# Performance work log

Measured on AMD Instinct MI355X. Metric: run time of the kernel, lower is better.

The kernel has to match this reference:

```python
import jax, jax.numpy as jnp
import numpy as np

B, T, C, H = 4, 2048, 768, 12
D = C // H  # head dim = 64


def setup_inputs() -> dict:
    key = jax.random.key(0)
    k1, k2, k3, k4 = jax.random.split(key, 4)
    x = jax.random.normal(k1, (B, T, C), dtype=jnp.float32)
    attn_mask = jnp.ones((B, T), dtype=jnp.float32)
    layer_lambda = jax.random.uniform(k2, (H,), dtype=jnp.float32)
    W_attn = jax.random.normal(k3, (C, 3 * C), dtype=jnp.float32) * (1.0 / np.sqrt(C))
    W_proj = jax.random.normal(k4, (C, C), dtype=jnp.float32) * (1.0 / np.sqrt(C))
    return {"x": x, "attn_mask": attn_mask, "layer_lambda": layer_lambda,
            "W_attn": W_attn, "W_proj": W_proj}


def reference(x, attn_mask, layer_lambda, W_attn, W_proj):
    Bx, Tx, Cx = x.shape
    qkv = x @ W_attn                      # (B, T, 3C)
    q, k, v = jnp.split(qkv, 3, axis=2)
    # (B, H, T, D)
    q = q.reshape(Bx, Tx, H, D).transpose(0, 2, 1, 3)
    k = k.reshape(Bx, Tx, H, D).transpose(0, 2, 1, 3)
    v = v.reshape(Bx, Tx, H, D).transpose(0, 2, 1, 3)

    att = jnp.einsum('bhqd,bhkd->bhqk', q, k) / jnp.sqrt(jnp.float32(D))

    # log-scale bias: scale row q of scores by (1 + lambda_h * log(q+1))
    log_pos = jnp.log(jnp.arange(Tx, dtype=jnp.float32) + 1.0)  # (T,)
    scale = 1.0 + layer_lambda[None, :, None, None] * log_pos[None, None, :, None]
    att = att * scale

    causal = jnp.tril(jnp.ones((Tx, Tx), dtype=jnp.float32))            # (T, T)
    mask = causal[None, None, :, :] * attn_mask[:, None, None, :]       # (B,1,T,T)

    # relu_attention path: relu, mask, normalize by row sum
    att = jax.nn.relu(att) * mask
    att_weights = att / (att.sum(axis=-1, keepdims=True) + 1e-9)

    out = jnp.einsum('bhqk,bhkd->bhqd', att_weights, v)  # (B, H, T, D)
    out = out.transpose(0, 2, 1, 3).reshape(Bx, Tx, Cx)
    return out @ W_proj
```

## Files before the change

kernel.cpp:

```cpp
#include <hip/hip_runtime.h>
#include <cstddef>
#include <cstdint>

#define Bn 4
#define Tn 2048
#define Cn 768
#define Hn 12

typedef __attribute__((ext_vector_type(8))) short short8v;
typedef __attribute__((ext_vector_type(4))) float f32x4;
typedef unsigned short ushort_t;

struct us4 { unsigned short x, y, z, w; };

__device__ inline unsigned short f2bf(float f) {
  union { float f; unsigned u; } v; v.f = f;
  unsigned r = v.u + 0x7FFFu + ((v.u >> 16) & 1u);
  return (unsigned short)(r >> 16);
}
__device__ inline float bf2f(unsigned short u) {
  union { unsigned u; float f; } v; v.u = ((unsigned)u) << 16;
  return v.f;
}
__device__ inline unsigned cvt_pk_bf16(float lo, float hi) {
  unsigned r;
  asm("v_cvt_pk_bf16_f32 %0, %1, %2" : "=v"(r) : "v"(lo), "v"(hi));
  return r;
}

#define GLOAD_LDS16(gp, lp)                                                        \
  __builtin_amdgcn_global_load_lds(                                                \
      (const __attribute__((address_space(1))) void*)(gp),                         \
      (__attribute__((address_space(3))) void*)(lp), 16, 0, 0)

__global__ __launch_bounds__(256) void prep_all(
    const float* __restrict__ x, ushort_t* __restrict__ xh, ushort_t* __restrict__ xl,
    const float* __restrict__ Wa, ushort_t* __restrict__ WaTh,
    ushort_t* __restrict__ WaTl, const float* __restrict__ Wp,
    ushort_t* __restrict__ WpT) {
  __shared__ float t[64][65];
  const int blk = blockIdx.x;
  const int tid = threadIdx.x;
  if (blk < 6144) {
    const int i = blk * 256 + tid;
    float4 v = reinterpret_cast<const float4*>(x)[i];
    us4 h;
    h.x = f2bf(v.x); h.y = f2bf(v.y); h.z = f2bf(v.z); h.w = f2bf(v.w);
    reinterpret_cast<us4*>(xh)[i] = h;
    const int row = (i << 2) / Cn;
    if ((row & (Tn - 1)) < 256) {
      us4 l;
      l.x = f2bf(v.x - bf2f(h.x)); l.y = f2bf(v.y - bf2f(h.y));
      l.z = f2bf(v.z - bf2f(h.z)); l.w = f2bf(v.w - bf2f(h.w));
      reinterpret_cast<us4*>(xl)[i] = l;
    }
    return;
  }
  const int id2 = blk - 6144;
  const int cx  = id2 % 48;
  const int ry  = id2 / 48;
  const bool split = (cx < 36);
  const float* W = split ? Wa : Wp;
  ushort_t* WTh  = split ? WaTh : WpT;
  const int cols = split ? 3 * Cn : Cn;
  const int c0   = (split ? cx : (cx - 36)) * 64;
  const int r0   = ry * 64;
  const int rows = Cn;
  const int c4 = (tid & 15) << 2;
  #pragma unroll
  for (int rr = 0; rr < 4; ++rr) {
    int r = rr * 16 + (tid >> 4);
    float4 v = *reinterpret_cast<const float4*>(&W[(size_t)(r0 + r) * cols + c0 + c4]);
    t[r][c4] = v.x; t[r][c4 + 1] = v.y; t[r][c4 + 2] = v.z; t[r][c4 + 3] = v.w;
  }
  __syncthreads();
  const int r4 = (tid & 15) << 2;
  #pragma unroll
  for (int cc = 0; cc < 4; ++cc) {
    int c = cc * 16 + (tid >> 4);
    float v0 = t[r4][c], v1 = t[r4 + 1][c], v2 = t[r4 + 2][c], v3 = t[r4 + 3][c];
    us4 h;
    h.x = f2bf(v0); h.y = f2bf(v1); h.z = f2bf(v2); h.w = f2bf(v3);
    *reinterpret_cast<us4*>(&WTh[(size_t)(c0 + c) * rows + r0 + r4]) = h;
    if (split) {
      us4 l;
      l.x = f2bf(v0 - bf2f(h.x)); l.y = f2bf(v1 - bf2f(h.y));
      l.z = f2bf(v2 - bf2f(h.z)); l.w = f2bf(v3 - bf2f(h.w));
      *reinterpret_cast<us4*>(&WaTl[(size_t)(c0 + c) * rows + r0 + r4]) = l;
    }
  }
}

__global__ __launch_bounds__(256) void gemm_qkv_fused(
    const ushort_t* __restrict__ Ah, const ushort_t* __restrict__ Al,
    const ushort_t* __restrict__ Bh, const ushort_t* __restrict__ Bl,
    const float* __restrict__ lambda, const float* __restrict__ attn_mask,
    ushort_t* __restrict__ qhp, ushort_t* __restrict__ qlp,
    ushort_t* __restrict__ khp, ushort_t* __restrict__ klp,
    ushort_t* __restrict__ vtp) {
  constexpr int K = Cn, N = 3 * Cn;
  __shared__ ushort_t As[2][128 * 64];
  __shared__ ushort_t Bs[2][128 * 64];

  const int tid = threadIdx.x;
  const int w = tid >> 6;
  const int lane = tid & 63;
  const int lcol = lane & 15;
  const int g = lane >> 4;
  const int xcd = blockIdx.x & 7;
  const int pos = blockIdx.x >> 3;
  const bool comp = (pos < 12);
  int bm, bn;
  if (comp) {
    const int cid = xcd * 12 + pos;
    bm = (xcd >> 1) * Tn + (xcd & 1) * 128;
    bn = (cid % 12) * 128;
  } else {
    const int pid = xcd * 144 + (pos - 12);
    bm = (pid / 18) * 128;
    bn = (pid % 18) * 128;
  }
  const int wr = (w >> 1) * 64;
  const int wc = (w & 1) * 64;
  const int srow = tid >> 3;
  const int sslot = tid & 7;

  f32x4 acc[4][4];
  #pragma unroll
  for (int m = 0; m < 4; ++m)
    #pragma unroll
    for (int n = 0; n < 4; ++n)
      acc[m][n] = (f32x4){0.f, 0.f, 0.f, 0.f};

  auto STAGE_A = [&](int k0, int buf, const ushort_t* A) {
    #pragma unroll
    for (int i = 0; i < 4; ++i) {
      const int row = i * 32 + srow;
      const int kslot = sslot ^ (row & 7);
      GLOAD_LDS16(A + (size_t)(bm + row) * K + k0 + kslot * 8,
                  (char*)As[buf] + (size_t)(i * 256 + tid) * 16);
    }
  };
  auto STAGE_B = [&](int k0, int buf, const ushort_t* B) {
    #pragma unroll
    for (int i = 0; i < 4; ++i) {
      const int row = i * 32 + srow;
      const int kslot = sslot ^ (row & 7);
      GLOAD_LDS16(B + (size_t)(bn + row) * K + k0 + kslot * 8,
                  (char*)Bs[buf] + (size_t)(i * 256 + tid) * 16);
    }
  };

  const int nt = K >> 6;
  if (!comp) {
    STAGE_A(0, 0, Ah); STAGE_B(0, 0, Bh);
    __syncthreads();
    for (int t = 0; t < nt; ++t) {
      const int cur = t & 1;
      if (t + 1 < nt) { STAGE_A((t + 1) << 6, cur ^ 1, Ah); STAGE_B((t + 1) << 6, cur ^ 1, Bh); }
      #pragma unroll
      for (int kk = 0; kk < 2; ++kk) {
        short8v a0[4], b0[4];
        #pragma unroll
        for (int m = 0; m < 4; ++m) {
          int row = wr + m * 16 + lcol;
          a0[m] = *reinterpret_cast<const short8v*>(
              (const char*)As[cur] + row * 128 + (((kk * 4 + g) ^ (row & 7)) << 4));
        }
        #pragma unroll
        for (int n = 0; n < 4; ++n) {
          int row = wc + n * 16 + lcol;
          b0[n] = *reinterpret_cast<const short8v*>(
              (const char*)Bs[cur] + row * 128 + (((kk * 4 + g) ^ (row & 7)) << 4));
        }
        #pragma unroll
        for (int m = 0; m < 4; ++m)
          #pragma unroll
          for (int n = 0; n < 4; ++n)
            acc[m][n] = __builtin_amdgcn_mfma_f32_16x16x32_bf16(a0[m], b0[n], acc[m][n], 0, 0, 0);
      }
      __syncthreads();
    }
  } else {
    for (int t = 0; t < nt; ++t) {
      const int k0 = t << 6;
      __syncthreads();
      STAGE_A(k0, 0, Ah); STAGE_B(k0, 0, Bh);
      STAGE_A(k0, 1, Al); STAGE_B(k0, 1, Bl);
      __syncthreads();
      #pragma unroll
      for (int kk = 0; kk < 2; ++kk) {
        short8v a0[4], b0[4], a1[4], b1[4];
        #pragma unroll
        for (int m = 0; m < 4; ++m) {
          int row = wr + m * 16 + lcol;
          int off = row * 128 + (((kk * 4 + g) ^ (row & 7)) << 4);
          a0[m] = *reinterpret_cast<const short8v*>((const char*)As[0] + off);
          a1[m] = *reinterpret_cast<const short8v*>((const char*)As[1] + off);
        }
        #pragma unroll
        for (int n = 0; n < 4; ++n) {
          int row = wc + n * 16 + lcol;
          int off = row * 128 + (((kk * 4 + g) ^ (row & 7)) << 4);
          b0[n] = *reinterpret_cast<const short8v*>((const char*)Bs[0] + off);
          b1[n] = *reinterpret_cast<const short8v*>((const char*)Bs[1] + off);
        }
        #pragma unroll
        for (int m = 0; m < 4; ++m)
          #pragma unroll
          for (int n = 0; n < 4; ++n) {
            acc[m][n] = __builtin_amdgcn_mfma_f32_16x16x32_bf16(a0[m], b0[n], acc[m][n], 0, 0, 0);
            acc[m][n] = __builtin_amdgcn_mfma_f32_16x16x32_bf16(a0[m], b1[n], acc[m][n], 0, 0, 0);
            acc[m][n] = __builtin_amdgcn_mfma_f32_16x16x32_bf16(a1[m], b0[n], acc[m][n], 0, 0, 0);
          }
      }
    }
  }

  const int seg = bn / Cn;
  const int nloc_base = bn - seg * Cn + wc;
  #pragma unroll
  for (int m = 0; m < 4; ++m) {
    const int mg = bm + wr + m * 16 + g * 4;
    const int bidx = mg >> 11;
    const int tbase = mg & (Tn - 1);
    float lgt[4];
    if (seg == 0) {
      #pragma unroll
      for (int j = 0; j < 4; ++j) lgt[j] = logf((float)(tbase + j) + 1.0f);
    }
    float4 mk4;
    if (seg == 1) mk4 = *reinterpret_cast<const float4*>(&attn_mask[bidx * Tn + tbase]);
    const bool wqk = comp ? true : (tbase >= 256);
    #pragma unroll
    for (int n = 0; n < 4; ++n) {
      const int nloc = nloc_base + n * 16 + lcol;
      const int h = nloc >> 6;
      const int d = nloc & 63;
      const size_t bhh = (size_t)(bidx * Hn + h);
      if (seg == 0) {
        if (wqk) {
          const float lam = lambda[h];
          #pragma unroll
          for (int j = 0; j < 4; ++j) {
            float val = acc[m][n][j] * (0.125f * (1.0f + lam * lgt[j]));
            unsigned short hi = f2bf(val);
            size_t idx = (bhh * Tn + tbase + j) * 64 + d;
            qhp[idx] = hi;
            if (comp) qlp[idx] = f2bf(val - bf2f(hi));
          }
        }
      } else if (seg == 1) {
        if (wqk) {
          const float* mkp = &mk4.x;
          #pragma unroll
          for (int j = 0; j < 4; ++j) {
            float val = acc[m][n][j] * mkp[j];
            unsigned short hi = f2bf(val);
            size_t idx = (bhh * Tn + tbase + j) * 64 + d;
            khp[idx] = hi;
            if (comp) klp[idx] = f2bf(val - bf2f(hi));
          }
        }
      } else {
        const int kt_ = tbase >> 6;
        const int tl_ = tbase & 63;
        us4 pv;
        pv.x = f2bf(acc[m][n][0]); pv.y = f2bf(acc[m][n][1]);
        pv.z = f2bf(acc[m][n][2]); pv.w = f2bf(acc[m][n][3]);
        *reinterpret_cast<us4*>(
            &vtp[(((bhh * 32 + kt_) * 64 + d) << 6) + tl_]) = pv;
      }
    }
  }
}

__global__ __launch_bounds__(256) void gemm_proj(
    const ushort_t* __restrict__ Ah, const ushort_t* __restrict__ Bh,
    float* __restrict__ C) {
  constexpr int K = Cn, N = Cn, MT = 64;
  __shared__ ushort_t As[2][MT * 64];
  __shared__ ushort_t Bs[2][128 * 64];

  const int tid = threadIdx.x;
  const int w = tid >> 6;
  const int lane = tid & 63;
  const int lcol = lane & 15;
  const int g = lane >> 4;
  const int id = (blockIdx.x & 7) * (gridDim.x >> 3) + (blockIdx.x >> 3);
  const int bm = (id / 6) * MT;
  const int bn = (id % 6) * 128;
  const int wr = (w >> 1) * 32;
  const int wc = (w & 1) * 64;
  const int srow = tid >> 3;
  const int sslot = tid & 7;

  f32x4 acc[2][4];
  #pragma unroll
  for (int m = 0; m < 2; ++m)
    #pragma unroll
    for (int n = 0; n < 4; ++n)
      acc[m][n] = (f32x4){0.f, 0.f, 0.f, 0.f};

  auto STAGE_A = [&](int k0, int buf) {
    #pragma unroll
    for (int i = 0; i < 2; ++i) {
      const int row = i * 32 + srow;
      const int kslot = sslot ^ (row & 7);
      GLOAD_LDS16(Ah + (size_t)(bm + row) * K + k0 + kslot * 8,
                  (char*)As[buf] + (size_t)(i * 256 + tid) * 16);
    }
  };
  auto STAGE_B = [&](int k0, int buf) {
    #pragma unroll
    for (int i = 0; i < 4; ++i) {
      const int row = i * 32 + srow;
      const int kslot = sslot ^ (row & 7);
      GLOAD_LDS16(Bh + (size_t)(bn + row) * K + k0 + kslot * 8,
                  (char*)Bs[buf] + (size_t)(i * 256 + tid) * 16);
    }
  };

  const int nt = K >> 6;
  STAGE_A(0, 0); STAGE_B(0, 0);
  __syncthreads();
  for (int t = 0; t < nt; ++t) {
    const int cur = t & 1;
    if (t + 1 < nt) { STAGE_A((t + 1) << 6, cur ^ 1); STAGE_B((t + 1) << 6, cur ^ 1); }
    #pragma unroll
    for (int kk = 0; kk < 2; ++kk) {
      short8v a0[2], b0[4];
      #pragma unroll
      for (int m = 0; m < 2; ++m) {
        int row = wr + m * 16 + lcol;
        a0[m] = *reinterpret_cast<const short8v*>(
            (const char*)As[cur] + row * 128 + (((kk * 4 + g) ^ (row & 7)) << 4));
      }
      #pragma unroll
      for (int n = 0; n < 4; ++n) {
        int row = wc + n * 16 + lcol;
        b0[n] = *reinterpret_cast<const short8v*>(
            (const char*)Bs[cur] + row * 128 + (((kk * 4 + g) ^ (row & 7)) << 4));
      }
      #pragma unroll
      for (int m = 0; m < 2; ++m)
        #pragma unroll
        for (int n = 0; n < 4; ++n)
          acc[m][n] = __builtin_amdgcn_mfma_f32_16x16x32_bf16(a0[m], b0[n], acc[m][n], 0, 0, 0);
    }
    __syncthreads();
  }

  #pragma unroll
  for (int m = 0; m < 2; ++m) {
    const int rowm = bm + wr + m * 16 + g * 4;
    #pragma unroll
    for (int n = 0; n < 4; ++n) {
      const int col = bn + wc + n * 16 + lcol;
      #pragma unroll
      for (int j = 0; j < 4; ++j)
        C[(size_t)(rowm + j) * N + col] = acc[m][n][j];
    }
  }
}

__global__ __launch_bounds__(256) void attn_mfma(
    const ushort_t* __restrict__ qh, const ushort_t* __restrict__ ql,
    const ushort_t* __restrict__ kh, const ushort_t* __restrict__ kl,
    const ushort_t* __restrict__ vt, ushort_t* __restrict__ ao) {
  const int xcd = blockIdx.x & 7;
  const int idx = blockIdx.x >> 3;
  const int bh  = xcd * 6 + (idx % 6);
  const int pr  = idx / 6;
  const int b = bh / Hn, h = bh % Hn;
  const int tid = threadIdx.x;
  const int w = tid >> 6, lane = tid & 63, lcol = lane & 15, g = lane >> 4;

  __shared__ ushort_t Kh_lds[2][64 * 64];
  __shared__ ushort_t V_lds[2][64 * 64];
  __shared__ ushort_t P_lds[4][16 * 64];

  for (int segq = 0; segq < 2; ++segq) {
    const int qt = segq ? (31 - pr) : pr;
    const bool compq = (qt <= 3);

    const size_t qoff0 = ((size_t)bh * Tn + qt * 64 + w * 16 + lcol) * 64;
    short8v qfh0 = *reinterpret_cast<const short8v*>(qh + qoff0 + g * 8);
    short8v qfh1 = *reinterpret_cast<const short8v*>(qh + qoff0 + 32 + g * 8);

    f32x4 o[4];
    #pragma unroll
    for (int dt = 0; dt < 4; ++dt) o[dt] = (f32x4){0.f, 0.f, 0.f, 0.f};
    float dsum = 0.f;

    auto STAGE = [&](int kt, int d) {
      const ushort_t* ks = kh + ((size_t)bh * Tn + kt * 64) * 64;
      const ushort_t* vs = vt + ((size_t)bh * 32 + kt) * 64 * 64;
      #pragma unroll
      for (int it = 0; it < 2; ++it) {
        const int s = it * 256 + tid;
        const int row = s >> 3, sslot = s & 7;
        const int swz = (sslot ^ (row & 7)) * 8;
        GLOAD_LDS16(ks + row * 64 + swz, (char*)Kh_lds[d] + (size_t)s * 16);
        GLOAD_LDS16(vs + row * 64 + swz, (char*)V_lds[d] + (size_t)s * 16);
      }
    };
    auto STAGE_KL = [&](int kt) {
      const ushort_t* ls = kl + ((size_t)bh * Tn + kt * 64) * 64;
      #pragma unroll
      for (int it = 0; it < 2; ++it) {
        const int s = it * 256 + tid;
        const int row = s >> 3, sslot = s & 7;
        const int swz = (sslot ^ (row & 7)) * 8;
        GLOAD_LDS16(ls + row * 64 + swz, (char*)Kh_lds[1] + (size_t)s * 16);
      }
    };

    auto COMPUTE = [&](int kt, int d, bool cq, bool ck) {
      const bool diag = (kt == qt);
      const int qr = qt * 64 + w * 16 + lcol;
      short8v qfl0, qfl1;
      if (cq) {
        qfl0 = *reinterpret_cast<const short8v*>(ql + qoff0 + g * 8);
        qfl1 = *reinterpret_cast<const short8v*>(ql + qoff0 + 32 + g * 8);
      }
      char* pb = (char*)P_lds[w];
      const int pswz = (lcol & 7) << 4;
      #pragma unroll
      for (int c = 0; c < 4; ++c) {
        const int row = c * 16 + lcol;
        const int roff = row * 128;
        const int s0 = (g ^ (row & 7)) << 4;
        const int s1 = ((4 + g) ^ (row & 7)) << 4;
        short8v kf0 = *reinterpret_cast<const short8v*>((const char*)Kh_lds[d] + roff + s0);
        short8v kf1 = *reinterpret_cast<const short8v*>((const char*)Kh_lds[d] + roff + s1);
        f32x4 s = (f32x4){0.f, 0.f, 0.f, 0.f};
        __builtin_amdgcn_s_setprio(1);
        s = __builtin_amdgcn_mfma_f32_16x16x32_bf16(kf0, qfh0, s, 0, 0, 0);
        s = __builtin_amdgcn_mfma_f32_16x16x32_bf16(kf1, qfh1, s, 0, 0, 0);
        if (cq) {
          s = __builtin_amdgcn_mfma_f32_16x16x32_bf16(kf0, qfl0, s, 0, 0, 0);
          s = __builtin_amdgcn_mfma_f32_16x16x32_bf16(kf1, qfl1, s, 0, 0, 0);
        }
        if (ck) {
          short8v kl0 = *reinterpret_cast<const short8v*>((const char*)Kh_lds[1] + roff + s0);
          short8v kl1 = *reinterpret_cast<const short8v*>((const char*)Kh_lds[1] + roff + s1);
          s = __builtin_amdgcn_mfma_f32_16x16x32_bf16(kl0, qfh0, s, 0, 0, 0);
          s = __builtin_amdgcn_mfma_f32_16x16x32_bf16(kl1, qfh1, s, 0, 0, 0);
        }
        __builtin_amdgcn_s_setprio(0);
        float sv[4];
        if (diag) {
          #pragma unroll
          for (int r = 0; r < 4; ++r) {
            float v = fmaxf(s[r], 0.f);
            const int kr = kt * 64 + c * 16 + g * 4 + r;
            sv[r] = (kr <= qr) ? v : 0.f;
          }
        } else {
          #pragma unroll
          for (int r = 0; r < 4; ++r) sv[r] = fmaxf(s[r], 0.f);
        }
        const unsigned p01 = cvt_pk_bf16(sv[0], sv[1]);
        const unsigned p23 = cvt_pk_bf16(sv[2], sv[3]);
        *reinterpret_cast<uint2*>(pb + lcol * 128 + ((c * 32 + g * 8) ^ pswz)) =
            make_uint2(p01, p23);
        dsum += (sv[0] + sv[1]) + (sv[2] + sv[3]);
      }
      short8v pf0 = *reinterpret_cast<const short8v*>(pb + lcol * 128 + ((g * 16) ^ pswz));
      short8v pf1 = *reinterpret_cast<const short8v*>(pb + lcol * 128 + ((64 + g * 16) ^ pswz));
      __builtin_amdgcn_s_setprio(1);
      #pragma unroll
      for (int dt = 0; dt < 4; ++dt) {
        const int vrow = dt * 16 + lcol;
        const int vro = vrow * 128;
        short8v vf0 = *reinterpret_cast<const short8v*>(
            (const char*)V_lds[d] + vro + ((g ^ (vrow & 7)) << 4));
        short8v vf1 = *reinterpret_cast<const short8v*>(
            (const char*)V_lds[d] + vro + (((4 + g) ^ (vrow & 7)) << 4));
        o[dt] = __builtin_amdgcn_mfma_f32_16x16x32_bf16(pf0, vf0, o[dt], 0, 0, 0);
        o[dt] = __builtin_amdgcn_mfma_f32_16x16x32_bf16(pf1, vf1, o[dt], 0, 0, 0);
      }
      __builtin_amdgcn_s_setprio(0);
    };

    if (qt <= 1) {
      for (int kt = 0; kt <= qt; ++kt) {
        STAGE(kt, 0);
        STAGE_KL(kt);
        __syncthreads();
        COMPUTE(kt, 0, true, true);
        __syncthreads();
      }
    } else {
      const int ntiles = qt + 1;
      STAGE(0, 0);
      __syncthreads();
      for (int kt = 0; kt < ntiles; ++kt) {
        const int d = kt & 1;
        if (kt + 1 < ntiles) STAGE(kt + 1, d ^ 1);
        COMPUTE(kt, d, compq, false);
        __syncthreads();
      }
    }

    float dtot = dsum;
    dtot += __shfl_xor(dtot, 16);
    dtot += __shfl_xor(dtot, 32);
    const float invq = 1.0f / (dtot + 1e-9f);
    float invs[4];
    #pragma unroll
    for (int r = 0; r < 4; ++r) invs[r] = __shfl(invq, g * 4 + r);

    ushort_t* ob = ao + ((size_t)b * Tn + qt * 64 + w * 16) * Cn + h * 64;
    #pragma unroll
    for (int dt = 0; dt < 4; ++dt)
      #pragma unroll
      for (int r = 0; r < 4; ++r)
        ob[(size_t)(g * 4 + r) * Cn + dt * 16 + lcol] = f2bf(o[dt][r] * invs[r]);
  }
}

extern "C" void kernel_launch(void* const* d_in, const int* in_sizes, int n_in,
                              void* d_out, int out_size, void* d_ws, size_t ws_size,
                              hipStream_t stream) {
  const float* x         = (const float*)d_in[0];
  const float* attn_mask = (const float*)d_in[1];
  const float* lambda    = (const float*)d_in[2];
  const float* W_attn    = (const float*)d_in[3];
  const float* W_proj    = (const float*)d_in[4];
  float* out = (float*)d_out;

  const size_t nBTC = (size_t)Bn * Tn * Cn;
  const size_t nW1  = (size_t)Cn * 3 * Cn;
  const size_t nW2  = (size_t)Cn * Cn;
  ushort_t* xh  = (ushort_t*)d_ws;
  ushort_t* xl  = xh + nBTC;
  ushort_t* WhT = xl + nBTC;
  ushort_t* WlT = WhT + nW1;
  ushort_t* WpT = WlT + nW1;
  ushort_t* qh  = WpT + nW2;
  ushort_t* ql  = qh + nBTC;
  ushort_t* kh  = ql + nBTC;
  ushort_t* kl  = kh + nBTC;
  ushort_t* vt  = kl + nBTC;
  ushort_t* ao  = xh;

  dim3 blk(256);

  prep_all<<<dim3(6720), blk, 0, stream>>>(
      x, xh, xl, W_attn, WhT, WlT, W_proj, WpT);

  gemm_qkv_fused<<<dim3(1248), blk, 0, stream>>>(
      xh, xl, WhT, WlT, lambda, attn_mask, qh, ql, kh, kl, vt);

  attn_mfma<<<dim3(768), blk, 0, stream>>>(
      qh, ql, kh, kl, vt, ao);

  gemm_proj<<<dim3(768), blk, 0, stream>>>(ao, WpT, out);
}
```

Measured before the change: 128.7 us.

## Share K/V tile staging between paired query tiles and reorder block scheduling

For query-tile pairs where neither tile needs the low-precision compensation path (pr > 3), the two tiles qt and 31-qt are now processed in a single pass over the K/V tiles. Each staged K/V tile is reused by both, which halves LDS staging and the barriers for the shorter tile. Blocks are also remapped so that the pairs needing compensation and the others are interleaved in a chosen order, aiming to balance the load. The cost is extra registers for two sets of accumulators and Q fragments, which may reduce occupancy.

```diff
diff --git a/kernel.cpp b/kernel.cpp
--- a/kernel.cpp
+++ b/kernel.cpp
@@ -370,8 +370,11 @@
     const ushort_t* __restrict__ vt, ushort_t* __restrict__ ao) {
   const int xcd = blockIdx.x & 7;
   const int idx = blockIdx.x >> 3;
-  const int bh  = xcd * 6 + (idx % 6);
-  const int pr  = idx / 6;
+  const int t_  = idx >> 5;
+  const int s_  = idx & 31;
+  const int j   = (t_ == 0) ? s_ : (t_ == 1 ? 32 + s_ : 95 - s_);
+  const int bh  = xcd * 6 + (j % 6);
+  const int pr  = j / 6;
   const int b = bh / Hn, h = bh % Hn;
   const int tid = threadIdx.x;
   const int w = tid >> 6, lane = tid & 63, lcol = lane & 15, g = lane >> 4;
@@ -380,144 +383,175 @@
   __shared__ ushort_t V_lds[2][64 * 64];
   __shared__ ushort_t P_lds[4][16 * 64];
 
-  for (int segq = 0; segq < 2; ++segq) {
-    const int qt = segq ? (31 - pr) : pr;
-    const bool compq = (qt <= 3);
-
-    const size_t qoff0 = ((size_t)bh * Tn + qt * 64 + w * 16 + lcol) * 64;
-    short8v qfh0 = *reinterpret_cast<const short8v*>(qh + qoff0 + g * 8);
-    short8v qfh1 = *reinterpret_cast<const short8v*>(qh + qoff0 + 32 + g * 8);
-
-    f32x4 o[4];
-    #pragma unroll
-    for (int dt = 0; dt < 4; ++dt) o[dt] = (f32x4){0.f, 0.f, 0.f, 0.f};
-    float dsum = 0.f;
-
-    auto STAGE = [&](int kt, int d) {
-      const ushort_t* ks = kh + ((size_t)bh * Tn + kt * 64) * 64;
-      const ushort_t* vs = vt + ((size_t)bh * 32 + kt) * 64 * 64;
-      #pragma unroll
-      for (int it = 0; it < 2; ++it) {
-        const int s = it * 256 + tid;
-        const int row = s >> 3, sslot = s & 7;
-        const int swz = (sslot ^ (row & 7)) * 8;
-        GLOAD_LDS16(ks + row * 64 + swz, (char*)Kh_lds[d] + (size_t)s * 16);
-        GLOAD_LDS16(vs + row * 64 + swz, (char*)V_lds[d] + (size_t)s * 16);
-      }
-    };
-    auto STAGE_KL = [&](int kt) {
-      const ushort_t* ls = kl + ((size_t)bh * Tn + kt * 64) * 64;
-      #pragma unroll
-      for (int it = 0; it < 2; ++it) {
-        const int s = it * 256 + tid;
-        const int row = s >> 3, sslot = s & 7;
-        const int swz = (sslot ^ (row & 7)) * 8;
-        GLOAD_LDS16(ls + row * 64 + swz, (char*)Kh_lds[1] + (size_t)s * 16);
-      }
-    };
-
-    auto COMPUTE = [&](int kt, int d, bool cq, bool ck) {
-      const bool diag = (kt == qt);
-      const int qr = qt * 64 + w * 16 + lcol;
-      short8v qfl0, qfl1;
+  char* pb = (char*)P_lds[w];
+  const int pswz = (lcol & 7) << 4;
+
+  auto STAGE = [&](int kt, int d) {
+    const ushort_t* ks = kh + ((size_t)bh * Tn + kt * 64) * 64;
+    const ushort_t* vs = vt + ((size_t)bh * 32 + kt) * 64 * 64;
+    #pragma unroll
+    for (int it = 0; it < 2; ++it) {
+      const int s = it * 256 + tid;
+      const int row = s >> 3, sslot = s & 7;
+      const int swz = (sslot ^ (row & 7)) * 8;
+      GLOAD_LDS16(ks + row * 64 + swz, (char*)Kh_lds[d] + (size_t)s * 16);
+      GLOAD_LDS16(vs + row * 64 + swz, (char*)V_lds[d] + (size_t)s * 16);
+    }
+  };
+  auto STAGE_KL = [&](int kt) {
+    const ushort_t* ls = kl + ((size_t)bh * Tn + kt * 64) * 64;
+    #pragma unroll
+    for (int it = 0; it < 2; ++it) {
+      const int s = it * 256 + tid;
+      const int row = s >> 3, sslot = s & 7;
+      const int swz = (sslot ^ (row & 7)) * 8;
+      GLOAD_LDS16(ls + row * 64 + swz, (char*)Kh_lds[1] + (size_t)s * 16);
+    }
+  };
+
+  auto QKPV = [&](int kt, int d, int qt_, size_t qoff_, short8v qf0, short8v qf1,
+                  bool cq, bool ck, f32x4 (&o_)[4], float& ds_) {
+    const bool diag = (kt == qt_);
+    const int qr = qt_ * 64 + w * 16 + lcol;
+    short8v qfl0, qfl1;
+    if (cq) {
+      qfl0 = *reinterpret_cast<const short8v*>(ql + qoff_ + g * 8);
+      qfl1 = *reinterpret_cast<const short8v*>(ql + qoff_ + 32 + g * 8);
+    }
+    #pragma unroll
+    for (int c = 0; c < 4; ++c) {
+      const int row = c * 16 + lcol;
+      const int roff = row * 128;
+      const int s0 = (g ^ (row & 7)) << 4;
+      const int s1 = ((4 + g) ^ (row & 7)) << 4;
+      short8v kf0 = *reinterpret_cast<const short8v*>((const char*)Kh_lds[d] + roff + s0);
+      short8v kf1 = *reinterpret_cast<const short8v*>((const char*)Kh_lds[d] + roff + s1);
+      f32x4 s = (f32x4){0.f, 0.f, 0.f, 0.f};
+      __builtin_amdgcn_s_setprio(1);
+      s = __builtin_amdgcn_mfma_f32_16x16x32_bf16(kf0, qf0, s, 0, 0, 0);
+      s = __builtin_amdgcn_mfma_f32_16x16x32_bf16(kf1, qf1, s, 0, 0, 0);
       if (cq) {
-        qfl0 = *reinterpret_cast<const short8v*>(ql + qoff0 + g * 8);
-        qfl1 = *reinterpret_cast<const short8v*>(ql + qoff0 + 32 + g * 8);
-      }
-      char* pb = (char*)P_lds[w];
-      const int pswz = (lcol & 7) << 4;
-      #pragma unroll
-      for (int c = 0; c < 4; ++c) {
-        const int row = c * 16 + lcol;
-        const int roff = row * 128;
-        const int s0 = (g ^ (row & 7)) << 4;
-        const int s1 = ((4 + g) ^ (row & 7)) << 4;
-        short8v kf0 = *reinterpret_cast<const short8v*>((const char*)Kh_lds[d] + roff + s0);
-        short8v kf1 = *reinterpret_cast<const short8v*>((const char*)Kh_lds[d] + roff + s1);
-        f32x4 s = (f32x4){0.f, 0.f, 0.f, 0.f};
-        __builtin_amdgcn_s_setprio(1);
-        s = __builtin_amdgcn_mfma_f32_16x16x32_bf16(kf0, qfh0, s, 0, 0, 0);
-        s = __builtin_amdgcn_mfma_f32_16x16x32_bf16(kf1, qfh1, s, 0, 0, 0);
-        if (cq) {
-          s = __builtin_amdgcn_mfma_f32_16x16x32_bf16(kf0, qfl0, s, 0, 0, 0);
-          s = __builtin_amdgcn_mfma_f32_16x16x32_bf16(kf1, qfl1, s, 0, 0, 0);
-        }
-        if (ck) {
-          short8v kl0 = *reinterpret_cast<const short8v*>((const char*)Kh_lds[1] + roff + s0);
-          short8v kl1 = *reinterpret_cast<const short8v*>((const char*)Kh_lds[1] + roff + s1);
-          s = __builtin_amdgcn_mfma_f32_16x16x32_bf16(kl0, qfh0, s, 0, 0, 0);
-          s = __builtin_amdgcn_mfma_f32_16x16x32_bf16(kl1, qfh1, s, 0, 0, 0);
-        }
-        __builtin_amdgcn_s_setprio(0);
-        float sv[4];
-        if (diag) {
-          #pragma unroll
-          for (int r = 0; r < 4; ++r) {
-            float v = fmaxf(s[r], 0.f);
-            const int kr = kt * 64 + c * 16 + g * 4 + r;
-            sv[r] = (kr <= qr) ? v : 0.f;
-          }
-        } else {
-          #pragma unroll
-          for (int r = 0; r < 4; ++r) sv[r] = fmaxf(s[r], 0.f);
-        }
-        const unsigned p01 = cvt_pk_bf16(sv[0], sv[1]);
-        const unsigned p23 = cvt_pk_bf16(sv[2], sv[3]);
-        *reinterpret_cast<uint2*>(pb + lcol * 128 + ((c * 32 + g * 8) ^ pswz)) =
-            make_uint2(p01, p23);
-        dsum += (sv[0] + sv[1]) + (sv[2] + sv[3]);
-      }
-      short8v pf0 = *reinterpret_cast<const short8v*>(pb + lcol * 128 + ((g * 16) ^ pswz));
-      short8v pf1 = *reinterpret_cast<const short8v*>(pb + lcol * 128 + ((64 + g * 16) ^ pswz));
-      __builtin_amdgcn_s_setprio(1);
-      #pragma unroll
-      for (int dt = 0; dt < 4; ++dt) {
-        const int vrow = dt * 16 + lcol;
-        const int vro = vrow * 128;
-        short8v vf0 = *reinterpret_cast<const short8v*>(
-            (const char*)V_lds[d] + vro + ((g ^ (vrow & 7)) << 4));
-        short8v vf1 = *reinterpret_cast<const short8v*>(
-            (const char*)V_lds[d] + vro + (((4 + g) ^ (vrow & 7)) << 4));
-        o[dt] = __builtin_amdgcn_mfma_f32_16x16x32_bf16(pf0, vf0, o[dt], 0, 0, 0);
-        o[dt] = __builtin_amdgcn_mfma_f32_16x16x32_bf16(pf1, vf1, o[dt], 0, 0, 0);
+        s = __builtin_amdgcn_mfma_f32_16x16x32_bf16(kf0, qfl0, s, 0, 0, 0);
+        s = __builtin_amdgcn_mfma_f32_16x16x32_bf16(kf1, qfl1, s, 0, 0, 0);
+      }
+      if (ck) {
+        short8v kl0 = *reinterpret_cast<const short8v*>((const char*)Kh_lds[1] + roff + s0);
+        short8v kl1 = *reinterpret_cast<const short8v*>((const char*)Kh_lds[1] + roff + s1);
+        s = __builtin_amdgcn_mfma_f32_16x16x32_bf16(kl0, qf0, s, 0, 0, 0);
+        s = __builtin_amdgcn_mfma_f32_16x16x32_bf16(kl1, qf1, s, 0, 0, 0);
       }
       __builtin_amdgcn_s_setprio(0);
-    };
-
-    if (qt <= 1) {
-      for (int kt = 0; kt <= qt; ++kt) {
-        STAGE(kt, 0);
-        STAGE_KL(kt);
-        __syncthreads();
-        COMPUTE(kt, 0, true, true);
-        __syncthreads();
-      }
-    } else {
-      const int ntiles = qt + 1;
-      STAGE(0, 0);
-      __syncthreads();
-      for (int kt = 0; kt < ntiles; ++kt) {
-        const int d = kt & 1;
-        if (kt + 1 < ntiles) STAGE(kt + 1, d ^ 1);
-        COMPUTE(kt, d, compq, false);
-        __syncthreads();
-      }
-    }
-
-    float dtot = dsum;
+      float sv[4];
+      if (diag) {
+        #pragma unroll
+        for (int r = 0; r < 4; ++r) {
+          float v = fmaxf(s[r], 0.f);
+          const int kr = kt * 64 + c * 16 + g * 4 + r;
+          sv[r] = (kr <= qr) ? v : 0.f;
+        }
+      } else {
+        #pragma unroll
+        for (int r = 0; r < 4; ++r) sv[r] = fmaxf(s[r], 0.f);
+      }
+      const unsigned p01 = cvt_pk_bf16(sv[0], sv[1]);
+      const unsigned p23 = cvt_pk_bf16(sv[2], sv[3]);
+      *reinterpret_cast<uint2*>(pb + lcol * 128 + ((c * 32 + g * 8) ^ pswz)) =
+          make_uint2(p01, p23);
+      ds_ += (sv[0] + sv[1]) + (sv[2] + sv[3]);
+    }
+    short8v pf0 = *reinterpret_cast<const short8v*>(pb + lcol * 128 + ((g * 16) ^ pswz));
+    short8v pf1 = *reinterpret_cast<const short8v*>(pb + lcol * 128 + ((64 + g * 16) ^ pswz));
+    __builtin_amdgcn_s_setprio(1);
+    #pragma unroll
+    for (int dt = 0; dt < 4; ++dt) {
+      const int vrow = dt * 16 + lcol;
+      const int vro = vrow * 128;
+      short8v vf0 = *reinterpret_cast<const short8v*>(
+          (const char*)V_lds[d] + vro + ((g ^ (vrow & 7)) << 4));
+      short8v vf1 = *reinterpret_cast<const short8v*>(
+          (const char*)V_lds[d] + vro + (((4 + g) ^ (vrow & 7)) << 4));
+      o_[dt] = __builtin_amdgcn_mfma_f32_16x16x32_bf16(pf0, vf0, o_[dt], 0, 0, 0);
+      o_[dt] = __builtin_amdgcn_mfma_f32_16x16x32_bf16(pf1, vf1, o_[dt], 0, 0, 0);
+    }
+    __builtin_amdgcn_s_setprio(0);
+  };
+
+  auto WRITEOUT = [&](int qt_, f32x4 (&o_)[4], float ds_) {
+    float dtot = ds_;
     dtot += __shfl_xor(dtot, 16);
     dtot += __shfl_xor(dtot, 32);
     const float invq = 1.0f / (dtot + 1e-9f);
     float invs[4];
     #pragma unroll
     for (int r = 0; r < 4; ++r) invs[r] = __shfl(invq, g * 4 + r);
-
-    ushort_t* ob = ao + ((size_t)b * Tn + qt * 64 + w * 16) * Cn + h * 64;
+    ushort_t* ob = ao + ((size_t)b * Tn + qt_ * 64 + w * 16) * Cn + h * 64;
     #pragma unroll
     for (int dt = 0; dt < 4; ++dt)
       #pragma unroll
       for (int r = 0; r < 4; ++r)
-        ob[(size_t)(g * 4 + r) * Cn + dt * 16 + lcol] = f2bf(o[dt][r] * invs[r]);
+        ob[(size_t)(g * 4 + r) * Cn + dt * 16 + lcol] = f2bf(o_[dt][r] * invs[r]);
+  };
+
+  if (pr <= 3) {
+    for (int segq = 0; segq < 2; ++segq) {
+      const int qt = segq ? (31 - pr) : pr;
+      const bool compq = (qt <= 3);
+      const size_t qoff0 = ((size_t)bh * Tn + qt * 64 + w * 16 + lcol) * 64;
+      short8v qfh0 = *reinterpret_cast<const short8v*>(qh + qoff0 + g * 8);
+      short8v qfh1 = *reinterpret_cast<const short8v*>(qh + qoff0 + 32 + g * 8);
+      f32x4 o[4];
+      #pragma unroll
+      for (int dt = 0; dt < 4; ++dt) o[dt] = (f32x4){0.f, 0.f, 0.f, 0.f};
+      float dsum = 0.f;
+      if (qt <= 1) {
+        for (int kt = 0; kt <= qt; ++kt) {
+          STAGE(kt, 0);
+          STAGE_KL(kt);
+          __syncthreads();
+          QKPV(kt, 0, qt, qoff0, qfh0, qfh1, true, true, o, dsum);
+          __syncthreads();
+        }
+      } else {
+        const int ntiles = qt + 1;
+        STAGE(0, 0);
+        __syncthreads();
+        for (int kt = 0; kt < ntiles; ++kt) {
+          const int d = kt & 1;
+          if (kt + 1 < ntiles) STAGE(kt + 1, d ^ 1);
+          QKPV(kt, d, qt, qoff0, qfh0, qfh1, compq, false, o, dsum);
+          __syncthreads();
+        }
+      }
+      WRITEOUT(qt, o, dsum);
+    }
+  } else {
+    const int qtA = pr, qtB = 31 - pr;
+    const size_t qoffA = ((size_t)bh * Tn + qtA * 64 + w * 16 + lcol) * 64;
+    const size_t qoffB = ((size_t)bh * Tn + qtB * 64 + w * 16 + lcol) * 64;
+    short8v qfA0 = *reinterpret_cast<const short8v*>(qh + qoffA + g * 8);
+    short8v qfA1 = *reinterpret_cast<const short8v*>(qh + qoffA + 32 + g * 8);
+    short8v qfB0 = *reinterpret_cast<const short8v*>(qh + qoffB + g * 8);
+    short8v qfB1 = *reinterpret_cast<const short8v*>(qh + qoffB + 32 + g * 8);
+    f32x4 oA[4], oB[4];
+    #pragma unroll
+    for (int dt = 0; dt < 4; ++dt) {
+      oA[dt] = (f32x4){0.f, 0.f, 0.f, 0.f};
+      oB[dt] = (f32x4){0.f, 0.f, 0.f, 0.f};
+    }
+    float dsA = 0.f, dsB = 0.f;
+    const int nt_ = qtB + 1;
+    STAGE(0, 0);
+    __syncthreads();
+    for (int kt = 0; kt < nt_; ++kt) {
+      const int d = kt & 1;
+      if (kt + 1 < nt_) STAGE(kt + 1, d ^ 1);
+      QKPV(kt, d, qtB, qoffB, qfB0, qfB1, false, false, oB, dsB);
+      if (kt <= qtA)
+        QKPV(kt, d, qtA, qoffA, qfA0, qfA1, false, false, oA, dsA);
+      __syncthreads();
+    }
+    WRITEOUT(qtA, oA, dsA);
+    WRITEOUT(qtB, oB, dsB);
   }
 }
 
```

Result: slower. 143.3 us (+11.3%).
